# Performance work log

Hardware: AMD Instinct MI355X
Metric: run time of the kernel (lower is better)

Reference implementation:

```python
import jax, jax.numpy as jnp
import numpy as np

N = 100000   # nodes
E = 1000000  # edges (before self-loops)
D = 64       # input_dim
H = 64       # hidden_dim
OUT = 8      # output_dim
G = 128      # num graphs in batch


def setup_inputs() -> dict:
    key = jax.random.key(0)
    ks = jax.random.split(key, 8)
    x = jax.random.normal(ks[0], (N, D), jnp.float32)
    edge_index = jax.random.randint(ks[1], (2, E), 0, N)
    edge_attr = jax.random.uniform(ks[2], (E,), jnp.float32)
    batch = jnp.sort(jax.random.randint(ks[3], (N,), 0, G))
    W1 = jax.random.normal(ks[4], (H, D), jnp.float32) / np.float32(np.sqrt(D))
    b1 = jnp.zeros((H,), jnp.float32)
    W2 = jax.random.normal(ks[5], (OUT, H), jnp.float32) / np.float32(np.sqrt(H))
    b2 = jnp.zeros((OUT,), jnp.float32)
    Wopt = jax.random.normal(ks[6], (1, H), jnp.float32) / np.float32(np.sqrt(H))
    bopt = jnp.zeros((1,), jnp.float32)
    return dict(x=x, edge_index=edge_index, edge_attr=edge_attr, batch=batch,
                W1=W1, b1=b1, W2=W2, b2=b2, Wopt=Wopt, bopt=bopt,
                num_graphs=G)


def gcn_conv(x, edge_index, edge_attr, W, b):
    n = x.shape[0]
    loop = jnp.arange(n)
    # add_self_loops with fill_value=1.0
    row = jnp.concatenate([edge_index[0], loop])
    col = jnp.concatenate([edge_index[1], loop])
    ea = jnp.concatenate([edge_attr, jnp.ones((n,), x.dtype)])
    # degree over row (source); >=1 because of self-loops
    deg = jax.ops.segment_sum(jnp.ones(row.shape, x.dtype), row, num_segments=n)
    dis = deg ** -0.5
    norm = dis[row] * dis[col]
    # message: edge_attr * x_j * norm, gathered from source row
    msg = (ea * norm)[:, None] * x[row]          # [E+N, D]
    aggr = jax.ops.segment_sum(msg, col, num_segments=n)  # scatter-add at target
    return aggr @ W.T + b                        # update: linear


def reference(x, edge_index, edge_attr, batch, W1, b1, W2, b2, Wopt, bopt, num_graphs):
    h = jnp.tanh(gcn_conv(x, edge_index, edge_attr, W1, b1))
    out = jax.nn.sigmoid(h @ W2.T + b2)          # [N, OUT]
    counts = jax.ops.segment_sum(jnp.ones((h.shape[0],), h.dtype), batch,
                                 num_segments=num_graphs)
    gemb = jax.ops.segment_sum(h, batch, num_segments=num_graphs)
    gemb = gemb / jnp.maximum(counts, 1.0)[:, None]  # global_mean_pool
    optimal = jax.nn.sigmoid(gemb @ Wopt.T + bopt)   # [G, 1]
    return (out, optimal)
```

## Files before the change

### kernel.cpp

```cpp
#include <hip/hip_runtime.h>
#include <math.h>
#include <stdint.h>

#define DD 64
#define HH 64
#define OUTD 8
#define NG 128
#define PSPLIT 8
#define NB 512
#define RSH 8
#define RMSK 255
#define CAPD 3072
#define BIN_CHUNK 4096
#define BT 1024

typedef short short8 __attribute__((ext_vector_type(8)));
typedef float f32x4 __attribute__((ext_vector_type(4)));

__device__ __forceinline__ float sigmoidf_(float v) { return 1.0f / (1.0f + __expf(-v)); }
__device__ __forceinline__ unsigned short f2bf(float f) {
    unsigned u = __float_as_uint(f);
    unsigned r = u + 0x7FFFu + ((u >> 16) & 1u);
    return (unsigned short)(r >> 16);
}
__device__ __forceinline__ float bf2f(unsigned short b) {
    return __uint_as_float(((unsigned)b) << 16);
}
__device__ __forceinline__ float bflo(unsigned q) { return __uint_as_float(q << 16); }
__device__ __forceinline__ float bfhi(unsigned q) { return __uint_as_float(q & 0xFFFF0000u); }

__device__ __forceinline__ int lbound_(const int* __restrict__ batch, int N, int g) {
    int lo = 0, hi = N;
    while (lo < hi) { int m = (lo + hi) >> 1; if (batch[m] < g) lo = m + 1; else hi = m; }
    return lo;
}

__global__ void init_kernel(int* cur2) {
    cur2[threadIdx.x] = 0;
}

__global__ __launch_bounds__(BT)
void bin_xcvt_kernel(const int* __restrict__ ei, const float* __restrict__ ea,
                     int* gcur, int* scur, int2* __restrict__ dreg,
                     unsigned char* __restrict__ sreg, int E, int nbin,
                     const float4* __restrict__ x4, uint4* __restrict__ xbf, int n8) {
    if (blockIdx.x >= nbin) {
        int i = (blockIdx.x - nbin) * BT + threadIdx.x;
        if (i < n8) {
            float4 a = x4[i * 2], b = x4[i * 2 + 1];
            uint4 o;
            o.x = (unsigned)f2bf(a.x) | ((unsigned)f2bf(a.y) << 16);
            o.y = (unsigned)f2bf(a.z) | ((unsigned)f2bf(a.w) << 16);
            o.z = (unsigned)f2bf(b.x) | ((unsigned)f2bf(b.y) << 16);
            o.w = (unsigned)f2bf(b.z) | ((unsigned)f2bf(b.w) << 16);
            xbf[i] = o;
        }
        return;
    }
    __shared__ int dcnt[NB], scnt[NB], dbase[NB], sbase[NB];
    int t = threadIdx.x;
    for (int j = t; j < NB; j += BT) { dcnt[j] = 0; scnt[j] = 0; }
    __syncthreads();
    int e0 = blockIdx.x * BIN_CHUNK;
    int lim = min(BIN_CHUNK, E - e0);
    int rv0 = 0, rv1 = 0, rv2 = 0, rv3 = 0;
    int cv0 = 0, cv1 = 0, cv2 = 0, cv3 = 0;
    float av0 = 0, av1 = 0, av2 = 0, av3 = 0;
    {
        int i;
        i = t;            if (i < lim) { rv0 = ei[e0+i]; cv0 = ei[E+e0+i]; av0 = ea[e0+i];
                                         atomicAdd(&dcnt[cv0 >> RSH], 1); atomicAdd(&scnt[rv0 >> RSH], 1); }
        i = t + BT;       if (i < lim) { rv1 = ei[e0+i]; cv1 = ei[E+e0+i]; av1 = ea[e0+i];
                                         atomicAdd(&dcnt[cv1 >> RSH], 1); atomicAdd(&scnt[rv1 >> RSH], 1); }
        i = t + 2 * BT;   if (i < lim) { rv2 = ei[e0+i]; cv2 = ei[E+e0+i]; av2 = ea[e0+i];
                                         atomicAdd(&dcnt[cv2 >> RSH], 1); atomicAdd(&scnt[rv2 >> RSH], 1); }
        i = t + 3 * BT;   if (i < lim) { rv3 = ei[e0+i]; cv3 = ei[E+e0+i]; av3 = ea[e0+i];
                                         atomicAdd(&dcnt[cv3 >> RSH], 1); atomicAdd(&scnt[rv3 >> RSH], 1); }
    }
    __syncthreads();
    for (int j = t; j < NB; j += BT) {
        int dc = dcnt[j], sc = scnt[j];
        dbase[j] = dc ? atomicAdd(&gcur[j], dc) : 0;
        sbase[j] = sc ? atomicAdd(&scur[j], sc) : 0;
        dcnt[j] = 0; scnt[j] = 0;
    }
    __syncthreads();
    #define EMIT(RR, CC, AA, II) do { \
        if ((II) < lim) { \
            int b_ = (CC) >> RSH, cl_ = (CC) & RMSK; \
            int pos_ = dbase[b_] + atomicAdd(&dcnt[b_], 1); \
            if (pos_ < CAPD) dreg[(size_t)b_ * CAPD + pos_] = make_int2((RR) | (cl_ << 20), __float_as_int(AA)); \
            int sb_ = (RR) >> RSH; \
            int sp_ = sbase[sb_] + atomicAdd(&scnt[sb_], 1); \
            if (sp_ < CAPD) sreg[(size_t)sb_ * CAPD + sp_] = (unsigned char)((RR) & RMSK); \
        } } while (0)
    EMIT(rv0, cv0, av0, t);
    EMIT(rv1, cv1, av1, t + BT);
    EMIT(rv2, cv2, av2, t + 2 * BT);
    EMIT(rv3, cv3, av3, t + 3 * BT);
    #undef EMIT
}

__global__ __launch_bounds__(256)
void deg_kernel(const unsigned char* __restrict__ sreg, const int* __restrict__ scur,
                float* __restrict__ dis, int N) {
    __shared__ int cnt[256];
    int t = threadIdx.x, b = blockIdx.x;
    cnt[t] = 0;
    __syncthreads();
    int n = min(scur[b], CAPD);
    const unsigned char* p = sreg + (size_t)b * CAPD;
    for (int i = t; i < n; i += 256) atomicAdd(&cnt[p[i]], 1);
    __syncthreads();
    int node = (b << RSH) + t;
    if (node < N) dis[node] = rsqrtf(1.0f + (float)cnt[t]);
}

__global__ __launch_bounds__(256)
void csr_kernel(int2* __restrict__ dreg, const int* __restrict__ gcur,
                const float* __restrict__ dis,
                int* __restrict__ colstart, int* __restrict__ colcnt, int N) {
    __shared__ int2 recs[CAPD];
    __shared__ int cnt[256], offs_s[256], sc[256];
    int t = threadIdx.x, b = blockIdx.x;
    int n = min(gcur[b], CAPD);
    size_t base = (size_t)b * CAPD;
    for (int i = t; i < n; i += 256) recs[i] = dreg[base + i];
    cnt[t] = 0;
    __syncthreads();
    for (int i = t; i < n; i += 256) atomicAdd(&cnt[recs[i].x >> 20], 1);
    __syncthreads();
    int my = cnt[t];
    sc[t] = my;
    __syncthreads();
    for (int off = 1; off < 256; off <<= 1) {
        int v = (t >= off) ? sc[t - off] : 0;
        __syncthreads();
        sc[t] += v;
        __syncthreads();
    }
    int ex = sc[t] - my;
    offs_s[t] = ex;
    int node = (b << RSH) + t;
    if (node < N) { colstart[node] = (int)(base + ex); colcnt[node] = my; }
    cnt[t] = 0;
    __syncthreads();
    for (int i = t; i < n; i += 256) {
        int2 rc = recs[i];
        int cl = rc.x >> 20;
        int r = rc.x & 0xFFFFF;
        float coef = __int_as_float(rc.y) * dis[r] * dis[(b << RSH) + cl];
        int pos = offs_s[cl] + atomicAdd(&cnt[cl], 1);
        dreg[base + pos] = make_int2(r, __float_as_int(coef));
    }
}

__global__ __launch_bounds__(256)
void gather_kernel(const int2* __restrict__ recs,
                   const int* __restrict__ colstart, const int* __restrict__ colcnt,
                   const float* __restrict__ dis,
                   const unsigned short* __restrict__ xbf,
                   unsigned* __restrict__ axb, int N) {
    int wid = blockIdx.x * 4 + (threadIdx.x >> 6);
    int l = threadIdx.x & 63;
    int q = l >> 4;
    int d4 = l & 15;
    int node = wid * 4 + q;
    bool v = node < N;
    float s = v ? dis[node] : 0.f;
    uint2 xv = v ? *(const uint2*)(xbf + (size_t)node * DD + 4 * d4) : make_uint2(0u, 0u);
    float s2 = s * s;
    float a0 = s2 * bflo(xv.x), a1 = s2 * bfhi(xv.x);
    float a2 = s2 * bflo(xv.y), a3 = s2 * bfhi(xv.y);
    float b0 = 0.f, b1 = 0.f, b2 = 0.f, b3 = 0.f;
    int cnt = v ? colcnt[node] : 0;
    const int2* p = recs + (v ? colstart[node] : 0);
    int k = 0;
    for (; k + 2 <= cnt; k += 2) {
        int2 r0 = p[k], r1 = p[k + 1];
        uint2 q0 = *(const uint2*)(xbf + (size_t)r0.x * DD + 4 * d4);
        uint2 q1 = *(const uint2*)(xbf + (size_t)r1.x * DD + 4 * d4);
        float c0 = __int_as_float(r0.y), c1 = __int_as_float(r1.y);
        a0 += c0 * bflo(q0.x); a1 += c0 * bfhi(q0.x);
        a2 += c0 * bflo(q0.y); a3 += c0 * bfhi(q0.y);
        b0 += c1 * bflo(q1.x); b1 += c1 * bfhi(q1.x);
        b2 += c1 * bflo(q1.y); b3 += c1 * bfhi(q1.y);
    }
    if (k < cnt) {
        int2 r0 = p[k];
        uint2 q0 = *(const uint2*)(xbf + (size_t)r0.x * DD + 4 * d4);
        float c0 = __int_as_float(r0.y);
        a0 += c0 * bflo(q0.x); a1 += c0 * bfhi(q0.x);
        a2 += c0 * bflo(q0.y); a3 += c0 * bfhi(q0.y);
    }
    if (v) {
        uint2 o;
        o.x = (unsigned)f2bf(a0 + b0) | ((unsigned)f2bf(a1 + b1) << 16);
        o.y = (unsigned)f2bf(a2 + b2) | ((unsigned)f2bf(a3 + b3) << 16);
        *(uint2*)(axb + (size_t)node * (DD / 2) + 2 * d4) = o;
    }
}

__global__ __launch_bounds__(256)
void head_kernel(const unsigned short* __restrict__ axb,
                 const float* __restrict__ W1, const float* __restrict__ b1,
                 const float* __restrict__ W2, const float* __restrict__ b2,
                 unsigned short* __restrict__ hb, float* __restrict__ outp, int N) {
    __shared__ __align__(16) float htile[4][16][68];
    int tid = threadIdx.x;
    int l = tid & 63, w = tid >> 6;
    int col = l & 15, kg = l >> 4;
    int half = l >> 5, d2 = l & 31;

    short8 w1f[4][2];
    #pragma unroll
    for (int ct = 0; ct < 4; ++ct)
        #pragma unroll
        for (int kt = 0; kt < 2; ++kt) {
            const float* src = W1 + (16 * ct + col) * DD + 32 * kt + 8 * kg;
            short8 f;
            #pragma unroll
            for (int j = 0; j < 8; ++j) f[j] = (short)f2bf(src[j]);
            w1f[ct][kt] = f;
        }
    short8 w2f[2];
    #pragma unroll
    for (int kt = 0; kt < 2; ++kt) {
        short8 f;
        #pragma unroll
        for (int j = 0; j < 8; ++j)
            f[j] = (col < OUTD) ? (short)f2bf(W2[col * HH + 32 * kt + 8 * kg + j]) : (short)0;
        w2f[kt] = f;
    }
    float b1v[4];
    #pragma unroll
    for (int ct = 0; ct < 4; ++ct) b1v[ct] = b1[16 * ct + col];
    float b2v = (col < OUTD) ? b2[col] : 0.f;

    int ngrp = (N + 15) >> 4;
    int g = blockIdx.x * 4 + w;
    bool act = g < ngrp;
    int base = act ? g * 16 : 0;
    int rr = min(base + col, N - 1);

    short8 af[2];
    #pragma unroll
    for (int kt = 0; kt < 2; ++kt)
        af[kt] = *(const short8*)(axb + (size_t)rr * DD + 32 * kt + 8 * kg);

    #pragma unroll
    for (int ct = 0; ct < 4; ++ct) {
        f32x4 acc = {0.f, 0.f, 0.f, 0.f};
        acc = __builtin_amdgcn_mfma_f32_16x16x32_bf16(af[0], w1f[ct][0], acc, 0, 0, 0);
        acc = __builtin_amdgcn_mfma_f32_16x16x32_bf16(af[1], w1f[ct][1], acc, 0, 0, 0);
        #pragma unroll
        for (int jr = 0; jr < 4; ++jr) {
            float v = acc[jr] + b1v[ct];
            float ez = __expf(2.f * v);
            htile[w][4 * kg + jr][16 * ct + col] = (ez - 1.f) / (ez + 1.f);
        }
    }
    __syncthreads();

    #pragma unroll
    for (int it = 0; it < 8; ++it) {
        int node = base + 2 * it + half;
        if (act && node < N) {
            float h0 = htile[w][2 * it + half][2 * d2];
            float h1 = htile[w][2 * it + half][2 * d2 + 1];
            *(unsigned*)(hb + (size_t)node * HH + 2 * d2) =
                (unsigned)f2bf(h0) | ((unsigned)f2bf(h1) << 16);
        }
    }

    short8 hf[2];
    #pragma unroll
    for (int kt = 0; kt < 2; ++kt) {
        const float* src = &htile[w][col][32 * kt + 8 * kg];
        float4 lo = *(const float4*)src;
        float4 hi = *(const float4*)(src + 4);
        short8 f;
        f[0] = (short)f2bf(lo.x); f[1] = (short)f2bf(lo.y);
        f[2] = (short)f2bf(lo.z); f[3] = (short)f2bf(lo.w);
        f[4] = (short)f2bf(hi.x); f[5] = (short)f2bf(hi.y);
        f[6] = (short)f2bf(hi.z); f[7] = (short)f2bf(hi.w);
        hf[kt] = f;
    }
    f32x4 acc2 = {0.f, 0.f, 0.f, 0.f};
    acc2 = __builtin_amdgcn_mfma_f32_16x16x32_bf16(hf[0], w2f[0], acc2, 0, 0, 0);
    acc2 = __builtin_amdgcn_mfma_f32_16x16x32_bf16(hf[1], w2f[1], acc2, 0, 0, 0);
    if (act && col < OUTD) {
        #pragma unroll
        for (int jr = 0; jr < 4; ++jr) {
            int node = base + 4 * kg + jr;
            if (node < N) outp[(size_t)node * OUTD + col] = sigmoidf_(acc2[jr] + b2v);
        }
    }
}

__global__ void pool_kernel(const unsigned short* __restrict__ hb,
                            const int* __restrict__ batch, int N,
                            float* __restrict__ pp) {
    int g = blockIdx.x / PSPLIT;
    int part = blockIdx.x % PSPLIT;
    int s = lbound_(batch, N, g);
    int e = lbound_(batch, N, g + 1);
    int tid = threadIdx.x;
    int hc = tid & 63, nl = tid >> 6;
    float sum = 0.0f;
    for (int n = s + part * 4 + nl; n < e; n += PSPLIT * 4)
        sum += bf2f(hb[(size_t)n * HH + hc]);
    __shared__ float red[4][HH];
    red[nl][hc] = sum;
    __syncthreads();
    if (nl == 0)
        pp[((size_t)g * PSPLIT + part) * HH + hc] =
            red[0][hc] + red[1][hc] + red[2][hc] + red[3][hc];
}

__global__ void optimal_kernel(const float* __restrict__ pp,
                               const int* __restrict__ batch, int N,
                               const float* __restrict__ Wopt,
                               const float* __restrict__ bopt,
                               float* __restrict__ out2) {
    int g = blockIdx.x;
    int d = threadIdx.x;
    int s = lbound_(batch, N, g);
    int e = lbound_(batch, N, g + 1);
    float c = fmaxf((float)(e - s), 1.0f);
    float acc = 0.f;
    #pragma unroll
    for (int part = 0; part < PSPLIT; ++part)
        acc += pp[((size_t)g * PSPLIT + part) * HH + d];
    float v = acc / c * Wopt[d];
    #pragma unroll
    for (int off = 32; off > 0; off >>= 1) v += __shfl_down(v, off);
    if (d == 0) out2[g] = 1.0f / (1.0f + __expf(-(v + bopt[0])));
}

extern "C" void kernel_launch(void* const* d_in, const int* in_sizes, int n_in,
                              void* d_out, int out_size, void* d_ws, size_t ws_size,
                              hipStream_t stream) {
    const float* x     = (const float*)d_in[0];
    const int*   ei    = (const int*)d_in[1];
    const float* ea    = (const float*)d_in[2];
    const int*   batch = (const int*)d_in[3];
    const float* W1    = (const float*)d_in[4];
    const float* b1    = (const float*)d_in[5];
    const float* W2    = (const float*)d_in[6];
    const float* b2    = (const float*)d_in[7];
    const float* Wopt  = (const float*)d_in[8];
    const float* bopt  = (const float*)d_in[9];

    int N = in_sizes[0] / DD;
    int E = in_sizes[2];
    int nbins = (N + 255) >> 8;

    float* out  = (float*)d_out;
    float* out2 = out + (size_t)N * OUTD;

    char* p = (char*)d_ws;
    float* dis      = (float*)p;  p += (size_t)N * 4;
    int*   colstart = (int*)p;    p += (size_t)N * 4;
    int*   colcnt   = (int*)p;    p += (size_t)N * 4;
    float* pp       = (float*)p;  p += (size_t)NG * PSPLIT * HH * 4;
    int*   gcur     = (int*)p;    p += (size_t)NB * 4;
    int*   scur     = (int*)p;    p += (size_t)NB * 4;
    uintptr_t up = (uintptr_t)p; up = (up + 15) & ~(uintptr_t)15; p = (char*)up;
    int2* dreg = (int2*)p;        p += (size_t)nbins * CAPD * 8;
    unsigned char* sreg = (unsigned char*)p; p += (size_t)nbins * CAPD;
    up = (uintptr_t)p; up = (up + 15) & ~(uintptr_t)15; p = (char*)up;
    unsigned short* xbf = (unsigned short*)p; p += (size_t)N * DD * 2;
    unsigned* axb = (unsigned*)p; p += (size_t)N * (DD / 2) * 4;
    unsigned short* hb  = (unsigned short*)p;

    int n8 = N * DD / 8;
    int nbin = (E + BIN_CHUNK - 1) / BIN_CHUNK;
    int nxc = (n8 + BT - 1) / BT;

    init_kernel<<<1, 2 * NB, 0, stream>>>(gcur);
    bin_xcvt_kernel<<<nbin + nxc, BT, 0, stream>>>(ei, ea, gcur, scur, dreg, sreg,
                                                   E, nbin,
                                                   (const float4*)x, (uint4*)xbf, n8);
    deg_kernel<<<nbins, 256, 0, stream>>>(sreg, scur, dis, N);
    csr_kernel<<<nbins, 256, 0, stream>>>(dreg, gcur, dis, colstart, colcnt, N);

    gather_kernel<<<(N + 15) / 16, 256, 0, stream>>>(dreg, colstart, colcnt, dis, xbf, axb, N);

    int ngrp = (N + 15) / 16;
    head_kernel<<<(ngrp + 3) / 4, 256, 0, stream>>>((const unsigned short*)axb,
                                                    W1, b1, W2, b2, hb, out, N);

    pool_kernel<<<NG * PSPLIT, 256, 0, stream>>>(hb, batch, N, pp);
    optimal_kernel<<<NG, 64, 0, stream>>>(pp, batch, N, Wopt, bopt, out2);
}
```

Before: 128.1 us.

## Fuse neighbor gather into MLP head kernel via shared-memory tiles

Merges the gather (SpMM aggregation) kernel with the head kernel so aggregated features stay in an LDS bf16 tile instead of a global round trip through axb. The gather now uses 8 lanes per node with 16-byte loads and 8 accumulators, and htile is stored as bf16 to shrink LDS traffic and allow 16-byte hb writes. This removes one kernel launch and the global write plus read of the aggregated tensor. In exchange, each wave holds gather state and MFMA weights together, which raises register pressure, and the lower latency hiding per node could hurt gather throughput. Drops the interleaved second accumulator set.

```diff
diff --git a/kernel.cpp b/kernel.cpp
--- a/kernel.cpp
+++ b/kernel.cpp
@@ -155,62 +155,20 @@
     }
 }
 
-__global__ __launch_bounds__(256)
-void gather_kernel(const int2* __restrict__ recs,
-                   const int* __restrict__ colstart, const int* __restrict__ colcnt,
-                   const float* __restrict__ dis,
-                   const unsigned short* __restrict__ xbf,
-                   unsigned* __restrict__ axb, int N) {
-    int wid = blockIdx.x * 4 + (threadIdx.x >> 6);
-    int l = threadIdx.x & 63;
-    int q = l >> 4;
-    int d4 = l & 15;
-    int node = wid * 4 + q;
-    bool v = node < N;
-    float s = v ? dis[node] : 0.f;
-    uint2 xv = v ? *(const uint2*)(xbf + (size_t)node * DD + 4 * d4) : make_uint2(0u, 0u);
-    float s2 = s * s;
-    float a0 = s2 * bflo(xv.x), a1 = s2 * bfhi(xv.x);
-    float a2 = s2 * bflo(xv.y), a3 = s2 * bfhi(xv.y);
-    float b0 = 0.f, b1 = 0.f, b2 = 0.f, b3 = 0.f;
-    int cnt = v ? colcnt[node] : 0;
-    const int2* p = recs + (v ? colstart[node] : 0);
-    int k = 0;
-    for (; k + 2 <= cnt; k += 2) {
-        int2 r0 = p[k], r1 = p[k + 1];
-        uint2 q0 = *(const uint2*)(xbf + (size_t)r0.x * DD + 4 * d4);
-        uint2 q1 = *(const uint2*)(xbf + (size_t)r1.x * DD + 4 * d4);
-        float c0 = __int_as_float(r0.y), c1 = __int_as_float(r1.y);
-        a0 += c0 * bflo(q0.x); a1 += c0 * bfhi(q0.x);
-        a2 += c0 * bflo(q0.y); a3 += c0 * bfhi(q0.y);
-        b0 += c1 * bflo(q1.x); b1 += c1 * bfhi(q1.x);
-        b2 += c1 * bflo(q1.y); b3 += c1 * bfhi(q1.y);
-    }
-    if (k < cnt) {
-        int2 r0 = p[k];
-        uint2 q0 = *(const uint2*)(xbf + (size_t)r0.x * DD + 4 * d4);
-        float c0 = __int_as_float(r0.y);
-        a0 += c0 * bflo(q0.x); a1 += c0 * bfhi(q0.x);
-        a2 += c0 * bflo(q0.y); a3 += c0 * bfhi(q0.y);
-    }
-    if (v) {
-        uint2 o;
-        o.x = (unsigned)f2bf(a0 + b0) | ((unsigned)f2bf(a1 + b1) << 16);
-        o.y = (unsigned)f2bf(a2 + b2) | ((unsigned)f2bf(a3 + b3) << 16);
-        *(uint2*)(axb + (size_t)node * (DD / 2) + 2 * d4) = o;
-    }
-}
-
-__global__ __launch_bounds__(256)
-void head_kernel(const unsigned short* __restrict__ axb,
-                 const float* __restrict__ W1, const float* __restrict__ b1,
-                 const float* __restrict__ W2, const float* __restrict__ b2,
-                 unsigned short* __restrict__ hb, float* __restrict__ outp, int N) {
-    __shared__ __align__(16) float htile[4][16][68];
+__global__ __launch_bounds__(256, 4)
+void ghead_kernel(const int2* __restrict__ recs,
+                  const int* __restrict__ colstart, const int* __restrict__ colcnt,
+                  const float* __restrict__ dis,
+                  const unsigned short* __restrict__ xbf,
+                  const float* __restrict__ W1, const float* __restrict__ b1,
+                  const float* __restrict__ W2, const float* __restrict__ b2,
+                  unsigned short* __restrict__ hb, float* __restrict__ outp, int N) {
+    __shared__ __align__(16) unsigned short atile[4][16][72];
+    __shared__ __align__(16) unsigned short htile[4][16][72];
     int tid = threadIdx.x;
     int l = tid & 63, w = tid >> 6;
     int col = l & 15, kg = l >> 4;
-    int half = l >> 5, d2 = l & 31;
+    int q = l >> 3, d8 = l & 7;
 
     short8 w1f[4][2];
     #pragma unroll
@@ -238,62 +196,89 @@
     float b2v = (col < OUTD) ? b2[col] : 0.f;
 
     int ngrp = (N + 15) >> 4;
-    int g = blockIdx.x * 4 + w;
-    bool act = g < ngrp;
-    int base = act ? g * 16 : 0;
-    int rr = min(base + col, N - 1);
-
-    short8 af[2];
-    #pragma unroll
-    for (int kt = 0; kt < 2; ++kt)
-        af[kt] = *(const short8*)(axb + (size_t)rr * DD + 32 * kt + 8 * kg);
-
-    #pragma unroll
-    for (int ct = 0; ct < 4; ++ct) {
-        f32x4 acc = {0.f, 0.f, 0.f, 0.f};
-        acc = __builtin_amdgcn_mfma_f32_16x16x32_bf16(af[0], w1f[ct][0], acc, 0, 0, 0);
-        acc = __builtin_amdgcn_mfma_f32_16x16x32_bf16(af[1], w1f[ct][1], acc, 0, 0, 0);
-        #pragma unroll
-        for (int jr = 0; jr < 4; ++jr) {
-            float v = acc[jr] + b1v[ct];
-            float ez = __expf(2.f * v);
-            htile[w][4 * kg + jr][16 * ct + col] = (ez - 1.f) / (ez + 1.f);
-        }
-    }
-    __syncthreads();
-
-    #pragma unroll
-    for (int it = 0; it < 8; ++it) {
-        int node = base + 2 * it + half;
-        if (act && node < N) {
-            float h0 = htile[w][2 * it + half][2 * d2];
-            float h1 = htile[w][2 * it + half][2 * d2 + 1];
-            *(unsigned*)(hb + (size_t)node * HH + 2 * d2) =
-                (unsigned)f2bf(h0) | ((unsigned)f2bf(h1) << 16);
-        }
-    }
-
-    short8 hf[2];
-    #pragma unroll
-    for (int kt = 0; kt < 2; ++kt) {
-        const float* src = &htile[w][col][32 * kt + 8 * kg];
-        float4 lo = *(const float4*)src;
-        float4 hi = *(const float4*)(src + 4);
-        short8 f;
-        f[0] = (short)f2bf(lo.x); f[1] = (short)f2bf(lo.y);
-        f[2] = (short)f2bf(lo.z); f[3] = (short)f2bf(lo.w);
-        f[4] = (short)f2bf(hi.x); f[5] = (short)f2bf(hi.y);
-        f[6] = (short)f2bf(hi.z); f[7] = (short)f2bf(hi.w);
-        hf[kt] = f;
-    }
-    f32x4 acc2 = {0.f, 0.f, 0.f, 0.f};
-    acc2 = __builtin_amdgcn_mfma_f32_16x16x32_bf16(hf[0], w2f[0], acc2, 0, 0, 0);
-    acc2 = __builtin_amdgcn_mfma_f32_16x16x32_bf16(hf[1], w2f[1], acc2, 0, 0, 0);
-    if (act && col < OUTD) {
-        #pragma unroll
-        for (int jr = 0; jr < 4; ++jr) {
-            int node = base + 4 * kg + jr;
-            if (node < N) outp[(size_t)node * OUTD + col] = sigmoidf_(acc2[jr] + b2v);
+    for (int grp = blockIdx.x * 4 + w; grp < ngrp; grp += gridDim.x * 4) {
+        int base = grp * 16;
+        #pragma unroll
+        for (int it = 0; it < 2; ++it) {
+            int node = base + it * 8 + q;
+            bool v = node < N;
+            float s = v ? dis[node] : 0.f;
+            uint4 xv = v ? *(const uint4*)(xbf + (size_t)node * DD + 8 * d8)
+                         : make_uint4(0u, 0u, 0u, 0u);
+            float s2 = s * s;
+            float a0 = s2 * bflo(xv.x), a1 = s2 * bfhi(xv.x);
+            float a2 = s2 * bflo(xv.y), a3 = s2 * bfhi(xv.y);
+            float a4 = s2 * bflo(xv.z), a5 = s2 * bfhi(xv.z);
+            float a6 = s2 * bflo(xv.w), a7 = s2 * bfhi(xv.w);
+            int cnt = v ? colcnt[node] : 0;
+            const int2* p = recs + (v ? colstart[node] : 0);
+            int k = 0;
+            for (; k + 2 <= cnt; k += 2) {
+                int2 r0 = p[k], r1 = p[k + 1];
+                uint4 q0 = *(const uint4*)(xbf + (size_t)r0.x * DD + 8 * d8);
+                uint4 q1 = *(const uint4*)(xbf + (size_t)r1.x * DD + 8 * d8);
+                float c0 = __int_as_float(r0.y), c1 = __int_as_float(r1.y);
+                a0 += c0 * bflo(q0.x); a1 += c0 * bfhi(q0.x);
+                a2 += c0 * bflo(q0.y); a3 += c0 * bfhi(q0.y);
+                a4 += c0 * bflo(q0.z); a5 += c0 * bfhi(q0.z);
+                a6 += c0 * bflo(q0.w); a7 += c0 * bfhi(q0.w);
+                a0 += c1 * bflo(q1.x); a1 += c1 * bfhi(q1.x);
+                a2 += c1 * bflo(q1.y); a3 += c1 * bfhi(q1.y);
+                a4 += c1 * bflo(q1.z); a5 += c1 * bfhi(q1.z);
+                a6 += c1 * bflo(q1.w); a7 += c1 * bfhi(q1.w);
+            }
+            if (k < cnt) {
+                int2 r0 = p[k];
+                uint4 q0 = *(const uint4*)(xbf + (size_t)r0.x * DD + 8 * d8);
+                float c0 = __int_as_float(r0.y);
+                a0 += c0 * bflo(q0.x); a1 += c0 * bfhi(q0.x);
+                a2 += c0 * bflo(q0.y); a3 += c0 * bfhi(q0.y);
+                a4 += c0 * bflo(q0.z); a5 += c0 * bfhi(q0.z);
+                a6 += c0 * bflo(q0.w); a7 += c0 * bfhi(q0.w);
+            }
+            uint4 o;
+            o.x = (unsigned)f2bf(a0) | ((unsigned)f2bf(a1) << 16);
+            o.y = (unsigned)f2bf(a2) | ((unsigned)f2bf(a3) << 16);
+            o.z = (unsigned)f2bf(a4) | ((unsigned)f2bf(a5) << 16);
+            o.w = (unsigned)f2bf(a6) | ((unsigned)f2bf(a7) << 16);
+            *(uint4*)&atile[w][it * 8 + q][8 * d8] = o;
+        }
+        short8 af[2];
+        #pragma unroll
+        for (int kt = 0; kt < 2; ++kt)
+            af[kt] = *(const short8*)&atile[w][col][32 * kt + 8 * kg];
+        #pragma unroll
+        for (int ct = 0; ct < 4; ++ct) {
+            f32x4 acc = {0.f, 0.f, 0.f, 0.f};
+            acc = __builtin_amdgcn_mfma_f32_16x16x32_bf16(af[0], w1f[ct][0], acc, 0, 0, 0);
+            acc = __builtin_amdgcn_mfma_f32_16x16x32_bf16(af[1], w1f[ct][1], acc, 0, 0, 0);
+            #pragma unroll
+            for (int jr = 0; jr < 4; ++jr) {
+                float v = acc[jr] + b1v[ct];
+                float ez = __expf(2.f * v);
+                htile[w][4 * kg + jr][16 * ct + col] = f2bf((ez - 1.f) / (ez + 1.f));
+            }
+        }
+        #pragma unroll
+        for (int it = 0; it < 2; ++it) {
+            int node = base + it * 8 + q;
+            if (node < N)
+                *(uint4*)(hb + (size_t)node * HH + 8 * d8) =
+                    *(const uint4*)&htile[w][it * 8 + q][8 * d8];
+        }
+        short8 hf[2];
+        #pragma unroll
+        for (int kt = 0; kt < 2; ++kt)
+            hf[kt] = *(const short8*)&htile[w][col][32 * kt + 8 * kg];
+        f32x4 acc2 = {0.f, 0.f, 0.f, 0.f};
+        acc2 = __builtin_amdgcn_mfma_f32_16x16x32_bf16(hf[0], w2f[0], acc2, 0, 0, 0);
+        acc2 = __builtin_amdgcn_mfma_f32_16x16x32_bf16(hf[1], w2f[1], acc2, 0, 0, 0);
+        if (col < OUTD) {
+            #pragma unroll
+            for (int jr = 0; jr < 4; ++jr) {
+                int node = base + 4 * kg + jr;
+                if (node < N) outp[(size_t)node * OUTD + col] = sigmoidf_(acc2[jr] + b2v);
+            }
         }
     }
 }
@@ -371,7 +356,6 @@
     unsigned char* sreg = (unsigned char*)p; p += (size_t)nbins * CAPD;
     up = (uintptr_t)p; up = (up + 15) & ~(uintptr_t)15; p = (char*)up;
     unsigned short* xbf = (unsigned short*)p; p += (size_t)N * DD * 2;
-    unsigned* axb = (unsigned*)p; p += (size_t)N * (DD / 2) * 4;
     unsigned short* hb  = (unsigned short*)p;
 
     int n8 = N * DD / 8;
@@ -385,11 +369,9 @@
     deg_kernel<<<nbins, 256, 0, stream>>>(sreg, scur, dis, N);
     csr_kernel<<<nbins, 256, 0, stream>>>(dreg, gcur, dis, colstart, colcnt, N);
 
-    gather_kernel<<<(N + 15) / 16, 256, 0, stream>>>(dreg, colstart, colcnt, dis, xbf, axb, N);
-
     int ngrp = (N + 15) / 16;
-    head_kernel<<<(ngrp + 3) / 4, 256, 0, stream>>>((const unsigned short*)axb,
-                                                    W1, b1, W2, b2, hb, out, N);
+    ghead_kernel<<<(ngrp + 3) / 4, 256, 0, stream>>>(dreg, colstart, colcnt, dis, xbf,
+                                                     W1, b1, W2, b2, hb, out, N);
 
     pool_kernel<<<NG * PSPLIT, 256, 0, stream>>>(hb, batch, N, pp);
     optimal_kernel<<<NG, 64, 0, stream>>>(pp, batch, N, Wopt, bopt, out2);
```

New measurement: 124.9 us. -2.5%, faster.
